# Performance work log

Measured on AMD Instinct MI355X. Metric: run time of the kernel, lower is better.

Reference implementation:

```python
import jax, jax.numpy as jnp
import numpy as np

B, V, S, E, K, FF = 16, 512, 1024, 8, 2, 2048  # batch, n_vars, seq_len, n_experts, top_k, ff_dim


def setup_inputs() -> dict:
    key = jax.random.key(0)
    ks = jax.random.split(key, 6)
    def w(k, shape, fan_in):
        return (jax.random.normal(k, shape, jnp.float32) / np.sqrt(fan_in)).astype(jnp.float32)
    return {
        "x": jax.random.normal(ks[0], (B, S, V), jnp.float32),
        "gate_W": w(ks[1], (E, S), S),          # Gating: Linear(seq_len -> n_experts), no bias
        "exp_W": w(ks[2], (E, S, S), S),        # per-expert Linear(seq_len -> seq_len) weights
        "exp_b": jnp.zeros((E, S), jnp.float32),
        "fc1_W": w(ks[3], (FF, V), V),          # MLPFeat fc1: Linear(n_vars -> ff_dim)
        "fc1_b": jnp.zeros((FF,), jnp.float32),
        "fc2_W": w(ks[4], (V, FF), FF),         # MLPFeat fc2: Linear(ff_dim -> n_vars)
        "fc2_b": jnp.zeros((V,), jnp.float32),
    }


def reference(x, gate_W, exp_W, exp_b, fc1_W, fc1_b, fc2_W, fc2_b):
    # Dropout layers are identity at inference.
    res = x                                   # [B,S,V]
    xt = jnp.swapaxes(x, 1, 2)                # [B,V,S] tokens of dim seq_len

    # --- MLPTime (multi_expert MoE) ---
    logits = jnp.einsum('bvs,es->bve', xt, gate_W)      # [B,V,E]
    probs = jax.nn.softmax(logits, axis=-1)             # gate_logits returned by torch code
    w, sel = jax.lax.top_k(probs, K)                    # [B,V,K]
    # combine top-k weights into a dense per-expert weight [B,V,E] (zeros off top-k)
    full_w = jnp.sum(jax.nn.one_hot(sel, E, dtype=xt.dtype) * w[..., None], axis=2)
    # all-expert outputs, then weighted combine (same math as the per-expert scatter loop)
    all_out = jnp.einsum('bvs,eos->bveo', xt, exp_W) + exp_b[None, None]  # [B,V,E,S]
    moe = jnp.einsum('bve,bveo->bvo', full_w, all_out)                    # [B,V,S]
    t = jax.nn.relu(moe)

    x = jnp.swapaxes(t, 1, 2) + res           # [B,S,V] residual

    # --- MLPFeat ---
    res2 = x
    h = jax.nn.relu(x @ fc1_W.T + fc1_b)      # [B,S,FF]
    x = h @ fc2_W.T + fc2_b + res2            # [B,S,V]
    return (x, probs)
```

## Files before the change

kernel.cpp:

```cpp
#include <hip/hip_runtime.h>
#include <stdint.h>

#define B_  16
#define V_  512
#define S_  1024
#define E_  8
#define FF_ 2048
#define NT_ (B_*V_)
#define NR_ (B_*S_)

typedef __attribute__((ext_vector_type(8))) short bf16x8;
typedef __attribute__((ext_vector_type(4))) float f32x4;

__device__ __forceinline__ unsigned short f2bf(float f) {
    unsigned int u = __float_as_uint(f);
    u += 0x7FFFu + ((u >> 16) & 1u);
    return (unsigned short)(u >> 16);
}
__device__ __forceinline__ float bf2f(unsigned short u) {
    return __uint_as_float(((unsigned int)u) << 16);
}

__device__ __forceinline__ void gl_lds16(const void* g, void* l) {
    __builtin_amdgcn_global_load_lds((const __attribute__((address_space(1))) void*)g,
                                     (__attribute__((address_space(3))) void*)l,
                                     16, 0, 0);
}

__global__ void k_f32_to_bf16(const float* __restrict__ src, unsigned short* __restrict__ dst, int n) {
    int i = (blockIdx.x * blockDim.x + threadIdx.x) * 4;
    if (i + 3 < n) {
        float4 v = *(const float4*)(src + i);
        ushort4 o; o.x = f2bf(v.x); o.y = f2bf(v.y); o.z = f2bf(v.z); o.w = f2bf(v.w);
        *(ushort4*)(dst + i) = o;
    } else {
        for (int j = i; j < n; ++j) dst[j] = f2bf(src[j]);
    }
}

__global__ void k_transpose_xt(const float* __restrict__ x, unsigned short* __restrict__ xt) {
    __shared__ float t[32][33];
    int b = blockIdx.z, st = blockIdx.y, vt = blockIdx.x;
    int col = threadIdx.x & 31, row8 = threadIdx.x >> 5;
    for (int r = 0; r < 4; ++r) {
        int sl = row8 + r * 8;
        t[sl][col] = x[(b * S_ + st * 32 + sl) * V_ + vt * 32 + col];
    }
    __syncthreads();
    for (int r = 0; r < 4; ++r) {
        int vl = row8 + r * 8;
        xt[(size_t)(b * V_ + vt * 32 + vl) * S_ + st * 32 + col] = f2bf(t[col][vl]);
    }
}

__global__ __launch_bounds__(256) void k_gate_part(const float* __restrict__ x,
                                                   const float* __restrict__ gate_W,
                                                   double* __restrict__ part,
                                                   int* __restrict__ cnt) {
    __shared__ float gw[E_ * 128];
    __shared__ double red[4 * 64 * E_];
    int sc = blockIdx.x, vt0 = blockIdx.y * 64, b = blockIdx.z;
    int tid = threadIdx.x;
    if (sc == 0 && blockIdx.y == 0 && b == 0 && tid < E_) cnt[tid] = 0;
    for (int i = tid; i < E_ * 128; i += 256) {
        int e = i >> 7, j = i & 127;
        gw[i] = gate_W[e * S_ + sc * 128 + j];
    }
    __syncthreads();
    int vl = tid & 63, sg = tid >> 6;
    double acc[E_];
    #pragma unroll
    for (int e = 0; e < E_; ++e) acc[e] = 0.0;
    for (int jj = sg; jj < 128; jj += 4) {
        int s = sc * 128 + jj;
        double xv = (double)x[(b * S_ + s) * V_ + vt0 + vl];
        #pragma unroll
        for (int e = 0; e < E_; ++e) acc[e] += xv * (double)gw[e * 128 + jj];
    }
    #pragma unroll
    for (int e = 0; e < E_; ++e) red[(sg * 64 + vl) * E_ + e] = acc[e];
    __syncthreads();
    for (int i = tid; i < 64 * E_; i += 256) {
        int tkn = i >> 3, e = i & 7;
        double s = red[(0 * 64 + tkn) * E_ + e] + red[(1 * 64 + tkn) * E_ + e]
                 + red[(2 * 64 + tkn) * E_ + e] + red[(3 * 64 + tkn) * E_ + e];
        int t = b * V_ + vt0 + tkn;
        part[((size_t)sc * NT_ + t) * E_ + e] = s;
    }
}

__global__ __launch_bounds__(256) void k_gate_fin(const double* __restrict__ part,
                                                  float* __restrict__ probs_out,
                                                  int* __restrict__ cnt, int* __restrict__ tok_of,
                                                  int* __restrict__ tk_slot, float* __restrict__ tk_w) {
    int t = blockIdx.x * 256 + threadIdx.x;
    int lane = threadIdx.x & 63;
    double l[E_];
    #pragma unroll
    for (int e = 0; e < E_; ++e) l[e] = 0.0;
    for (int c = 0; c < S_ / 128; ++c) {
        const double* p = part + ((size_t)c * NT_ + t) * E_;
        #pragma unroll
        for (int e = 0; e < E_; ++e) l[e] += p[e];
    }
    double m = l[0];
    #pragma unroll
    for (int e = 1; e < E_; ++e) m = l[e] > m ? l[e] : m;
    double p[E_], sum = 0.0;
    #pragma unroll
    for (int e = 0; e < E_; ++e) { p[e] = exp(l[e] - m); sum += p[e]; }
    float pf[E_];
    #pragma unroll
    for (int e = 0; e < E_; ++e) pf[e] = (float)(p[e] / sum);
    float4 pa = {pf[0], pf[1], pf[2], pf[3]}, pb = {pf[4], pf[5], pf[6], pf[7]};
    *(float4*)(probs_out + (size_t)t * E_) = pa;
    *(float4*)(probs_out + (size_t)t * E_ + 4) = pb;
    int i0 = 0;
    #pragma unroll
    for (int e = 1; e < E_; ++e) if (pf[e] > pf[i0]) i0 = e;
    int i1 = -1;
    #pragma unroll
    for (int e = 0; e < E_; ++e) if (e != i0 && (i1 < 0 || pf[e] > pf[i1])) i1 = e;
    int sel[2] = {i0, i1};
    float wsel[2] = {pf[i0], pf[i1]};
    #pragma unroll
    for (int k = 0; k < 2; ++k) {
        int ie = sel[k];
        int pos = 0;
        for (int e = 0; e < E_; ++e) {
            unsigned long long msk = __ballot(ie == e);
            if (ie == e) {
                int rank = __popcll(msk & ((1ull << lane) - 1ull));
                int leader = __ffsll((long long)msk) - 1;
                int base = 0;
                if (lane == leader) base = atomicAdd(&cnt[e], __popcll(msk));
                base = __shfl(base, leader);
                pos = base + rank;
            }
        }
        tok_of[ie * NT_ + pos] = t;
        tk_slot[t * 2 + k] = (ie << 16) | pos;
        tk_w[t * 2 + k] = wsel[k];
    }
}

__global__ void k_scan(const int* __restrict__ cnt, int* __restrict__ offs,
                       int* __restrict__ tile_hdr) {
    if (threadIdx.x == 0) {
        int o = 0, nt = 0;
        for (int e = 0; e < E_; ++e) {
            offs[e] = o;
            for (int p = 0; p < cnt[e]; p += 128) {
                tile_hdr[1 + nt * 2] = e;
                tile_hdr[2 + nt * 2] = p;
                ++nt;
            }
            o += cnt[e];
        }
        offs[E_] = o;
        tile_hdr[0] = nt;
    }
}

__device__ __forceinline__ void gemm_k_loop(const unsigned short* a0, const unsigned short* a1,
                                            const unsigned short* b0, const unsigned short* b1,
                                            short* As, short* Bs, int kIters, int wave, int lane,
                                            f32x4 (&acc)[4][4]) {
    char* ldsA = (char*)As + wave * 2048;
    char* ldsB = (char*)Bs + wave * 2048;
    int wm = (wave & 1) << 6, wn = (wave >> 1) << 6;
    int lr = lane & 15, quad = lane >> 4;
    for (int kk = 0; kk < kIters; ++kk) {
        gl_lds16(a0, ldsA);
        gl_lds16(a1, ldsA + 1024);
        gl_lds16(b0, ldsB);
        gl_lds16(b1, ldsB + 1024);
        a0 += 32; a1 += 32; b0 += 32; b1 += 32;
        __syncthreads();
        bf16x8 af[4], bfv[4];
        #pragma unroll
        for (int i = 0; i < 4; ++i)
            af[i] = *(const bf16x8*)(As + (wm + i * 16 + lr) * 32 + quad * 8);
        #pragma unroll
        for (int j = 0; j < 4; ++j)
            bfv[j] = *(const bf16x8*)(Bs + (wn + j * 16 + lr) * 32 + quad * 8);
        #pragma unroll
        for (int i = 0; i < 4; ++i)
            #pragma unroll
            for (int j = 0; j < 4; ++j)
                acc[i][j] = __builtin_amdgcn_mfma_f32_16x16x32_bf16(af[i], bfv[j], acc[i][j], 0, 0, 0);
        __syncthreads();
    }
}

__global__ __launch_bounds__(256) void k_moe_gemm(const unsigned short* __restrict__ xt,
                                                  const unsigned short* __restrict__ expWb,
                                                  const float* __restrict__ exp_b,
                                                  const int* __restrict__ cnt, const int* __restrict__ offs,
                                                  const int* __restrict__ tok_of,
                                                  const int* __restrict__ tile_hdr,
                                                  unsigned short* __restrict__ Yb) {
    int ntl = tile_hdr[0];
    if ((int)blockIdx.x >= ntl) return;
    int e    = tile_hdr[1 + blockIdx.x * 2];
    int pos0 = tile_hdr[2 + blockIdx.x * 2];
    int ne = cnt[e];
    int nt = blockIdx.y;
    __shared__ __align__(16) short As[128 * 32];
    __shared__ __align__(16) short Bs[128 * 32];
    int tid = threadIdx.x, wave = tid >> 6, lane = tid & 63;
    int rA0 = wave * 32 + (lane >> 2);
    int rA1 = rA0 + 16;
    int koff = (lane & 3) * 8;
    int tok0 = tok_of[e * NT_ + min(pos0 + rA0, ne - 1)];
    int tok1 = tok_of[e * NT_ + min(pos0 + rA1, ne - 1)];
    const unsigned short* a0 = xt + (size_t)tok0 * S_ + koff;
    const unsigned short* a1 = xt + (size_t)tok1 * S_ + koff;
    const unsigned short* Wb = expWb + (size_t)e * S_ * S_;
    const unsigned short* b0 = Wb + (size_t)(nt * 128 + rA0) * S_ + koff;
    const unsigned short* b1 = Wb + (size_t)(nt * 128 + rA1) * S_ + koff;
    f32x4 acc[4][4] = {};
    gemm_k_loop(a0, a1, b0, b1, As, Bs, S_ / 32, wave, lane, acc);
    int wm = (wave & 1) << 6, wn = (wave >> 1) << 6;
    int lr = lane & 15, quad = lane >> 4;
    int yrow0 = offs[e];
    #pragma unroll
    for (int i = 0; i < 4; ++i)
        #pragma unroll
        for (int r = 0; r < 4; ++r) {
            int pos = pos0 + wm + i * 16 + quad * 4 + r;
            if (pos < ne) {
                size_t row = (size_t)(yrow0 + pos);
                #pragma unroll
                for (int j = 0; j < 4; ++j) {
                    int col = nt * 128 + wn + j * 16 + lr;
                    Yb[row * S_ + col] = f2bf(acc[i][j][r] + exp_b[e * S_ + col]);
                }
            }
        }
}

__global__ void k_combine(const float* __restrict__ x, const unsigned short* __restrict__ Yb,
                          const int* __restrict__ offs, const int* __restrict__ tk_slot,
                          const float* __restrict__ tk_w,
                          unsigned short* __restrict__ x2b) {
    __shared__ float t[32][33];
    int b = blockIdx.z, st = blockIdx.y, vt = blockIdx.x;
    int tid = threadIdx.x;
    int vl = tid >> 3, sq = (tid & 7) * 4;
    int tok = b * V_ + vt * 32 + vl;
    int s0 = tk_slot[tok * 2 + 0], s1 = tk_slot[tok * 2 + 1];
    float w0 = tk_w[tok * 2 + 0], w1 = tk_w[tok * 2 + 1];
    size_t r0 = (size_t)(offs[s0 >> 16] + (s0 & 0xFFFF));
    size_t r1 = (size_t)(offs[s1 >> 16] + (s1 & 0xFFFF));
    int sg = st * 32 + sq;
    ushort4 y0 = *(const ushort4*)(Yb + r0 * S_ + sg);
    ushort4 y1 = *(const ushort4*)(Yb + r1 * S_ + sg);
    t[vl][sq + 0] = fmaxf(w0 * bf2f(y0.x) + w1 * bf2f(y1.x), 0.f);
    t[vl][sq + 1] = fmaxf(w0 * bf2f(y0.y) + w1 * bf2f(y1.y), 0.f);
    t[vl][sq + 2] = fmaxf(w0 * bf2f(y0.z) + w1 * bf2f(y1.z), 0.f);
    t[vl][sq + 3] = fmaxf(w0 * bf2f(y0.w) + w1 * bf2f(y1.w), 0.f);
    __syncthreads();
    int vcol = tid & 31, srow8 = tid >> 5;
    for (int r = 0; r < 4; ++r) {
        int sl = srow8 + r * 8;
        size_t gi = (size_t)(b * S_ + st * 32 + sl) * V_ + vt * 32 + vcol;
        x2b[gi] = f2bf(x[gi] + t[vcol][sl]);
    }
}

__global__ __launch_bounds__(256) void k_fc1(const unsigned short* __restrict__ x2b,
                                             const unsigned short* __restrict__ w1b,
                                             const float* __restrict__ fc1_b,
                                             unsigned short* __restrict__ h) {
    __shared__ __align__(16) short As[128 * 32];
    __shared__ __align__(16) short Bs[128 * 32];
    int tid = threadIdx.x, wave = tid >> 6, lane = tid & 63;
    int rA0 = wave * 32 + (lane >> 2), rA1 = rA0 + 16;
    int koff = (lane & 3) * 8;
    int m0 = blockIdx.x * 128, n0 = blockIdx.y * 128;
    const unsigned short* a0 = x2b + (size_t)(m0 + rA0) * V_ + koff;
    const unsigned short* a1 = x2b + (size_t)(m0 + rA1) * V_ + koff;
    const unsigned short* b0 = w1b + (size_t)(n0 + rA0) * V_ + koff;
    const unsigned short* b1 = w1b + (size_t)(n0 + rA1) * V_ + koff;
    f32x4 acc[4][4] = {};
    gemm_k_loop(a0, a1, b0, b1, As, Bs, V_ / 32, wave, lane, acc);
    int wm = (wave & 1) << 6, wn = (wave >> 1) << 6;
    int lr = lane & 15, quad = lane >> 4;
    #pragma unroll
    for (int i = 0; i < 4; ++i)
        #pragma unroll
        for (int r = 0; r < 4; ++r) {
            size_t row = (size_t)(m0 + wm + i * 16 + quad * 4 + r);
            #pragma unroll
            for (int j = 0; j < 4; ++j) {
                int col = n0 + wn + j * 16 + lr;
                h[row * FF_ + col] = f2bf(fmaxf(acc[i][j][r] + fc1_b[col], 0.f));
            }
        }
}

__global__ __launch_bounds__(256) void k_fc2(const unsigned short* __restrict__ h,
                                             const unsigned short* __restrict__ w2b,
                                             const float* __restrict__ fc2_b,
                                             const unsigned short* __restrict__ x2b,
                                             float* __restrict__ out) {
    __shared__ __align__(16) short As[128 * 32];
    __shared__ __align__(16) short Bs[128 * 32];
    int tid = threadIdx.x, wave = tid >> 6, lane = tid & 63;
    int rA0 = wave * 32 + (lane >> 2), rA1 = rA0 + 16;
    int koff = (lane & 3) * 8;
    int m0 = blockIdx.x * 128, n0 = blockIdx.y * 128;
    const unsigned short* a0 = h + (size_t)(m0 + rA0) * FF_ + koff;
    const unsigned short* a1 = h + (size_t)(m0 + rA1) * FF_ + koff;
    const unsigned short* b0 = w2b + (size_t)(n0 + rA0) * FF_ + koff;
    const unsigned short* b1 = w2b + (size_t)(n0 + rA1) * FF_ + koff;
    f32x4 acc[4][4] = {};
    gemm_k_loop(a0, a1, b0, b1, As, Bs, FF_ / 32, wave, lane, acc);
    int wm = (wave & 1) << 6, wn = (wave >> 1) << 6;
    int lr = lane & 15, quad = lane >> 4;
    #pragma unroll
    for (int i = 0; i < 4; ++i)
        #pragma unroll
        for (int r = 0; r < 4; ++r) {
            size_t row = (size_t)(m0 + wm + i * 16 + quad * 4 + r);
            #pragma unroll
            for (int j = 0; j < 4; ++j) {
                int col = n0 + wn + j * 16 + lr;
                out[row * V_ + col] = acc[i][j][r] + fc2_b[col] + bf2f(x2b[row * V_ + col]);
            }
        }
}

extern "C" void kernel_launch(void* const* d_in, const int* in_sizes, int n_in,
                              void* d_out, int out_size, void* d_ws, size_t ws_size,
                              hipStream_t stream) {
    const float* x      = (const float*)d_in[0];
    const float* gate_W = (const float*)d_in[1];
    const float* exp_W  = (const float*)d_in[2];
    const float* exp_b  = (const float*)d_in[3];
    const float* fc1_W  = (const float*)d_in[4];
    const float* fc1_b  = (const float*)d_in[5];
    const float* fc2_W  = (const float*)d_in[6];
    const float* fc2_b  = (const float*)d_in[7];
    float* out_x = (float*)d_out;
    float* out_p = (float*)d_out + (size_t)B_ * S_ * V_;

    if (ws_size < (size_t)155582592) return;

    char* ws = (char*)d_ws;
    unsigned short* Yb    = (unsigned short*)(ws);
    unsigned short* xt    = (unsigned short*)(ws +  67108864);
    int*            tile_hdr = (int*)(ws + 83886080);
    unsigned short* x2b   = (unsigned short*)(ws + 117440512);
    unsigned short* expWb = (unsigned short*)(ws + 134217728);
    unsigned short* fc1Wb = (unsigned short*)(ws + 150994944);
    unsigned short* fc2Wb = (unsigned short*)(ws + 153092096);
    char* route = ws + 155189248;
    int*   cnt     = (int*)(route);
    int*   offs    = (int*)(route + 64);
    int*   tok_of  = (int*)(route + 128);
    int*   tk_slot = (int*)(route + 128 + 262144);
    float* tk_w    = (float*)(route + 128 + 262144 + 65536);
    unsigned short* h = (unsigned short*)ws;
    double* part = (double*)ws;

    k_f32_to_bf16<<<dim3(8192), 256, 0, stream>>>(exp_W, expWb, E_ * S_ * S_);
    k_f32_to_bf16<<<dim3(1024), 256, 0, stream>>>(fc1_W, fc1Wb, FF_ * V_);
    k_f32_to_bf16<<<dim3(1024), 256, 0, stream>>>(fc2_W, fc2Wb, V_ * FF_);
    k_transpose_xt<<<dim3(V_ / 32, S_ / 32, B_), 256, 0, stream>>>(x, xt);
    k_gate_part<<<dim3(S_ / 128, V_ / 64, B_), 256, 0, stream>>>(x, gate_W, part, cnt);
    k_gate_fin<<<dim3(NT_ / 256), 256, 0, stream>>>(part, out_p, cnt, tok_of, tk_slot, tk_w);
    k_scan<<<1, 64, 0, stream>>>(cnt, offs, tile_hdr);
    k_moe_gemm<<<dim3(136, S_ / 128), 256, 0, stream>>>(xt, expWb, exp_b, cnt, offs, tok_of, tile_hdr, Yb);
    k_combine<<<dim3(V_ / 32, S_ / 32, B_), 256, 0, stream>>>(x, Yb, offs, tk_slot, tk_w, x2b);
    k_fc1<<<dim3(NR_ / 128, FF_ / 128), 256, 0, stream>>>(x2b, fc1Wb, fc1_b, h);
    k_fc2<<<dim3(NR_ / 128, V_ / 128), 256, 0, stream>>>(h, fc2Wb, fc2_b, x2b, out_x);
}
```

Baseline: 360.3 us.

## Widen MoE and fc1 GEMM tiles to 128x256 and fuse weight conversions

The GEMM k-loop becomes a template on the per-wave N width. The MoE expert GEMM and fc1 now use 128x256 output tiles, with each wave computing 64x128 from 4x8 MFMA accumulators and B-loaders reorganised to match. This raises reuse of the A tile per LDS load and halves the number of blocks that reload activations, at the cost of more accumulator registers, possible lower occupancy and fewer blocks to fill the CUs. The three separate f32-to-bf16 weight conversion launches are merged into one kernel to save launch overhead.

```diff
diff --git a/kernel.cpp b/kernel.cpp
--- a/kernel.cpp
+++ b/kernel.cpp
@@ -27,15 +27,18 @@
                                      16, 0, 0);
 }
 
-__global__ void k_f32_to_bf16(const float* __restrict__ src, unsigned short* __restrict__ dst, int n) {
-    int i = (blockIdx.x * blockDim.x + threadIdx.x) * 4;
-    if (i + 3 < n) {
-        float4 v = *(const float4*)(src + i);
-        ushort4 o; o.x = f2bf(v.x); o.y = f2bf(v.y); o.z = f2bf(v.z); o.w = f2bf(v.w);
-        *(ushort4*)(dst + i) = o;
-    } else {
-        for (int j = i; j < n; ++j) dst[j] = f2bf(src[j]);
-    }
+__device__ __forceinline__ void cvt4(const float* s, unsigned short* d, int i) {
+    float4 v = *(const float4*)(s + i);
+    ushort4 o; o.x = f2bf(v.x); o.y = f2bf(v.y); o.z = f2bf(v.z); o.w = f2bf(v.w);
+    *(ushort4*)(d + i) = o;
+}
+__global__ void k_convert3(const float* __restrict__ s0, unsigned short* __restrict__ d0, int g0,
+                           const float* __restrict__ s1, unsigned short* __restrict__ d1, int g1,
+                           const float* __restrict__ s2, unsigned short* __restrict__ d2) {
+    int g = blockIdx.x * 256 + threadIdx.x;
+    if (g < g0)           cvt4(s0, d0, g * 4);
+    else if (g < g0 + g1) cvt4(s1, d1, (g - g0) * 4);
+    else                  cvt4(s2, d2, (g - g0 - g1) * 4);
 }
 
 __global__ void k_transpose_xt(const float* __restrict__ x, unsigned short* __restrict__ xt) {
@@ -162,32 +165,36 @@
     }
 }
 
-__device__ __forceinline__ void gemm_k_loop(const unsigned short* a0, const unsigned short* a1,
-                                            const unsigned short* b0, const unsigned short* b1,
-                                            short* As, short* Bs, int kIters, int wave, int lane,
-                                            f32x4 (&acc)[4][4]) {
+template<int TN>
+__device__ __forceinline__ void gemm_k_loop_t(const unsigned short* a0, const unsigned short* a1,
+                                              const unsigned short* (&bp)[TN / 2],
+                                              short* As, short* Bs, int kIters, int wave, int lane,
+                                              f32x4 (&acc)[4][TN]) {
     char* ldsA = (char*)As + wave * 2048;
-    char* ldsB = (char*)Bs + wave * 2048;
-    int wm = (wave & 1) << 6, wn = (wave >> 1) << 6;
+    char* ldsB = (char*)Bs + wave * (TN / 2) * 1024;
+    int wm = (wave & 1) << 6;
+    int wn = (wave >> 1) * (TN * 16);
     int lr = lane & 15, quad = lane >> 4;
     for (int kk = 0; kk < kIters; ++kk) {
         gl_lds16(a0, ldsA);
         gl_lds16(a1, ldsA + 1024);
-        gl_lds16(b0, ldsB);
-        gl_lds16(b1, ldsB + 1024);
-        a0 += 32; a1 += 32; b0 += 32; b1 += 32;
+        #pragma unroll
+        for (int c = 0; c < TN / 2; ++c) gl_lds16(bp[c], ldsB + c * 1024);
+        a0 += 32; a1 += 32;
+        #pragma unroll
+        for (int c = 0; c < TN / 2; ++c) bp[c] += 32;
         __syncthreads();
-        bf16x8 af[4], bfv[4];
+        bf16x8 af[4], bfv[TN];
         #pragma unroll
         for (int i = 0; i < 4; ++i)
             af[i] = *(const bf16x8*)(As + (wm + i * 16 + lr) * 32 + quad * 8);
         #pragma unroll
-        for (int j = 0; j < 4; ++j)
+        for (int j = 0; j < TN; ++j)
             bfv[j] = *(const bf16x8*)(Bs + (wn + j * 16 + lr) * 32 + quad * 8);
         #pragma unroll
         for (int i = 0; i < 4; ++i)
             #pragma unroll
-            for (int j = 0; j < 4; ++j)
+            for (int j = 0; j < TN; ++j)
                 acc[i][j] = __builtin_amdgcn_mfma_f32_16x16x32_bf16(af[i], bfv[j], acc[i][j], 0, 0, 0);
         __syncthreads();
     }
@@ -205,9 +212,9 @@
     int e    = tile_hdr[1 + blockIdx.x * 2];
     int pos0 = tile_hdr[2 + blockIdx.x * 2];
     int ne = cnt[e];
-    int nt = blockIdx.y;
+    int n0 = blockIdx.y * 256;
     __shared__ __align__(16) short As[128 * 32];
-    __shared__ __align__(16) short Bs[128 * 32];
+    __shared__ __align__(16) short Bs[256 * 32];
     int tid = threadIdx.x, wave = tid >> 6, lane = tid & 63;
     int rA0 = wave * 32 + (lane >> 2);
     int rA1 = rA0 + 16;
@@ -217,11 +224,13 @@
     const unsigned short* a0 = xt + (size_t)tok0 * S_ + koff;
     const unsigned short* a1 = xt + (size_t)tok1 * S_ + koff;
     const unsigned short* Wb = expWb + (size_t)e * S_ * S_;
-    const unsigned short* b0 = Wb + (size_t)(nt * 128 + rA0) * S_ + koff;
-    const unsigned short* b1 = Wb + (size_t)(nt * 128 + rA1) * S_ + koff;
-    f32x4 acc[4][4] = {};
-    gemm_k_loop(a0, a1, b0, b1, As, Bs, S_ / 32, wave, lane, acc);
-    int wm = (wave & 1) << 6, wn = (wave >> 1) << 6;
+    const unsigned short* bp[4];
+    #pragma unroll
+    for (int c = 0; c < 4; ++c)
+        bp[c] = Wb + (size_t)(n0 + wave * 64 + c * 16 + (lane >> 2)) * S_ + koff;
+    f32x4 acc[4][8] = {};
+    gemm_k_loop_t<8>(a0, a1, bp, As, Bs, S_ / 32, wave, lane, acc);
+    int wm = (wave & 1) << 6, wn = (wave >> 1) << 7;
     int lr = lane & 15, quad = lane >> 4;
     int yrow0 = offs[e];
     #pragma unroll
@@ -232,8 +241,8 @@
             if (pos < ne) {
                 size_t row = (size_t)(yrow0 + pos);
                 #pragma unroll
-                for (int j = 0; j < 4; ++j) {
-                    int col = nt * 128 + wn + j * 16 + lr;
+                for (int j = 0; j < 8; ++j) {
+                    int col = n0 + wn + j * 16 + lr;
                     Yb[row * S_ + col] = f2bf(acc[i][j][r] + exp_b[e * S_ + col]);
                 }
             }
@@ -274,18 +283,20 @@
                                              const float* __restrict__ fc1_b,
                                              unsigned short* __restrict__ h) {
     __shared__ __align__(16) short As[128 * 32];
-    __shared__ __align__(16) short Bs[128 * 32];
+    __shared__ __align__(16) short Bs[256 * 32];
     int tid = threadIdx.x, wave = tid >> 6, lane = tid & 63;
     int rA0 = wave * 32 + (lane >> 2), rA1 = rA0 + 16;
     int koff = (lane & 3) * 8;
-    int m0 = blockIdx.x * 128, n0 = blockIdx.y * 128;
+    int m0 = blockIdx.x * 128, n0 = blockIdx.y * 256;
     const unsigned short* a0 = x2b + (size_t)(m0 + rA0) * V_ + koff;
     const unsigned short* a1 = x2b + (size_t)(m0 + rA1) * V_ + koff;
-    const unsigned short* b0 = w1b + (size_t)(n0 + rA0) * V_ + koff;
-    const unsigned short* b1 = w1b + (size_t)(n0 + rA1) * V_ + koff;
-    f32x4 acc[4][4] = {};
-    gemm_k_loop(a0, a1, b0, b1, As, Bs, V_ / 32, wave, lane, acc);
-    int wm = (wave & 1) << 6, wn = (wave >> 1) << 6;
+    const unsigned short* bp[4];
+    #pragma unroll
+    for (int c = 0; c < 4; ++c)
+        bp[c] = w1b + (size_t)(n0 + wave * 64 + c * 16 + (lane >> 2)) * V_ + koff;
+    f32x4 acc[4][8] = {};
+    gemm_k_loop_t<8>(a0, a1, bp, As, Bs, V_ / 32, wave, lane, acc);
+    int wm = (wave & 1) << 6, wn = (wave >> 1) << 7;
     int lr = lane & 15, quad = lane >> 4;
     #pragma unroll
     for (int i = 0; i < 4; ++i)
@@ -293,7 +304,7 @@
         for (int r = 0; r < 4; ++r) {
             size_t row = (size_t)(m0 + wm + i * 16 + quad * 4 + r);
             #pragma unroll
-            for (int j = 0; j < 4; ++j) {
+            for (int j = 0; j < 8; ++j) {
                 int col = n0 + wn + j * 16 + lr;
                 h[row * FF_ + col] = f2bf(fmaxf(acc[i][j][r] + fc1_b[col], 0.f));
             }
@@ -313,10 +324,12 @@
     int m0 = blockIdx.x * 128, n0 = blockIdx.y * 128;
     const unsigned short* a0 = h + (size_t)(m0 + rA0) * FF_ + koff;
     const unsigned short* a1 = h + (size_t)(m0 + rA1) * FF_ + koff;
-    const unsigned short* b0 = w2b + (size_t)(n0 + rA0) * FF_ + koff;
-    const unsigned short* b1 = w2b + (size_t)(n0 + rA1) * FF_ + koff;
+    const unsigned short* bp[2];
+    #pragma unroll
+    for (int c = 0; c < 2; ++c)
+        bp[c] = w2b + (size_t)(n0 + wave * 32 + c * 16 + (lane >> 2)) * FF_ + koff;
     f32x4 acc[4][4] = {};
-    gemm_k_loop(a0, a1, b0, b1, As, Bs, FF_ / 32, wave, lane, acc);
+    gemm_k_loop_t<4>(a0, a1, bp, As, Bs, FF_ / 32, wave, lane, acc);
     int wm = (wave & 1) << 6, wn = (wave >> 1) << 6;
     int lr = lane & 15, quad = lane >> 4;
     #pragma unroll
@@ -365,15 +378,14 @@
     unsigned short* h = (unsigned short*)ws;
     double* part = (double*)ws;
 
-    k_f32_to_bf16<<<dim3(8192), 256, 0, stream>>>(exp_W, expWb, E_ * S_ * S_);
-    k_f32_to_bf16<<<dim3(1024), 256, 0, stream>>>(fc1_W, fc1Wb, FF_ * V_);
-    k_f32_to_bf16<<<dim3(1024), 256, 0, stream>>>(fc2_W, fc2Wb, V_ * FF_);
+    k_convert3<<<dim3((2097152 + 262144 + 262144) / 256), 256, 0, stream>>>(
+        exp_W, expWb, 2097152, fc1_W, fc1Wb, 262144, fc2_W, fc2Wb);
     k_transpose_xt<<<dim3(V_ / 32, S_ / 32, B_), 256, 0, stream>>>(x, xt);
     k_gate_part<<<dim3(S_ / 128, V_ / 64, B_), 256, 0, stream>>>(x, gate_W, part, cnt);
     k_gate_fin<<<dim3(NT_ / 256), 256, 0, stream>>>(part, out_p, cnt, tok_of, tk_slot, tk_w);
     k_scan<<<1, 64, 0, stream>>>(cnt, offs, tile_hdr);
-    k_moe_gemm<<<dim3(136, S_ / 128), 256, 0, stream>>>(xt, expWb, exp_b, cnt, offs, tok_of, tile_hdr, Yb);
+    k_moe_gemm<<<dim3(135, S_ / 256), 256, 0, stream>>>(xt, expWb, exp_b, cnt, offs, tok_of, tile_hdr, Yb);
     k_combine<<<dim3(V_ / 32, S_ / 32, B_), 256, 0, stream>>>(x, Yb, offs, tk_slot, tk_w, x2b);
-    k_fc1<<<dim3(NR_ / 128, FF_ / 128), 256, 0, stream>>>(x2b, fc1Wb, fc1_b, h);
+    k_fc1<<<dim3(NR_ / 128, FF_ / 256), 256, 0, stream>>>(x2b, fc1Wb, fc1_b, h);
     k_fc2<<<dim3(NR_ / 128, V_ / 128), 256, 0, stream>>>(h, fc2Wb, fc2_b, x2b, out_x);
 }
```

After: 430.8 us. 19.6% more time.

## Switch GEMMs to 32x32x16 MFMA, merge weight conversions, add occupancy hints

Applied to the files above, without the earlier changes.

Replaces the 16x16x32 bf16 MFMA tiling in the shared GEMM inner loop with 32x32x16 MFMAs (2x2 per wave over two k-substeps). The epilogues of the MoE, fc1 and fc2 GEMMs are remapped to the new accumulator layout. The aim is fewer LDS fragment reads per FLOP and higher MFMA throughput. It also fuses the three fp32-to-bf16 weight conversion launches into one kernel, and adds launch_bounds occupancy hints to the MoE and fc1 kernels. The risk is register pressure from 4x16 accumulators under the occupancy hint, plus a changed LDS access pattern that may bank-conflict.

```diff
diff --git a/kernel.cpp b/kernel.cpp
--- a/kernel.cpp
+++ b/kernel.cpp
@@ -10,7 +10,7 @@
 #define NR_ (B_*S_)
 
 typedef __attribute__((ext_vector_type(8))) short bf16x8;
-typedef __attribute__((ext_vector_type(4))) float f32x4;
+typedef __attribute__((ext_vector_type(16))) float f32x16;
 
 __device__ __forceinline__ unsigned short f2bf(float f) {
     unsigned int u = __float_as_uint(f);
@@ -27,15 +27,18 @@
                                      16, 0, 0);
 }
 
-__global__ void k_f32_to_bf16(const float* __restrict__ src, unsigned short* __restrict__ dst, int n) {
-    int i = (blockIdx.x * blockDim.x + threadIdx.x) * 4;
-    if (i + 3 < n) {
-        float4 v = *(const float4*)(src + i);
-        ushort4 o; o.x = f2bf(v.x); o.y = f2bf(v.y); o.z = f2bf(v.z); o.w = f2bf(v.w);
-        *(ushort4*)(dst + i) = o;
-    } else {
-        for (int j = i; j < n; ++j) dst[j] = f2bf(src[j]);
-    }
+__device__ __forceinline__ void cvt4(const float* s, unsigned short* d, int i) {
+    float4 v = *(const float4*)(s + i);
+    ushort4 o; o.x = f2bf(v.x); o.y = f2bf(v.y); o.z = f2bf(v.z); o.w = f2bf(v.w);
+    *(ushort4*)(d + i) = o;
+}
+__global__ void k_convert3(const float* __restrict__ s0, unsigned short* __restrict__ d0, int g0,
+                           const float* __restrict__ s1, unsigned short* __restrict__ d1, int g1,
+                           const float* __restrict__ s2, unsigned short* __restrict__ d2) {
+    int g = blockIdx.x * 256 + threadIdx.x;
+    if (g < g0)           cvt4(s0, d0, g * 4);
+    else if (g < g0 + g1) cvt4(s1, d1, (g - g0) * 4);
+    else                  cvt4(s2, d2, (g - g0 - g1) * 4);
 }
 
 __global__ void k_transpose_xt(const float* __restrict__ x, unsigned short* __restrict__ xt) {
@@ -162,14 +165,14 @@
     }
 }
 
-__device__ __forceinline__ void gemm_k_loop(const unsigned short* a0, const unsigned short* a1,
-                                            const unsigned short* b0, const unsigned short* b1,
-                                            short* As, short* Bs, int kIters, int wave, int lane,
-                                            f32x4 (&acc)[4][4]) {
+__device__ __forceinline__ void gemm_k_loop32(const unsigned short* a0, const unsigned short* a1,
+                                              const unsigned short* b0, const unsigned short* b1,
+                                              short* As, short* Bs, int kIters, int wave, int lane,
+                                              f32x16 (&acc)[2][2]) {
     char* ldsA = (char*)As + wave * 2048;
     char* ldsB = (char*)Bs + wave * 2048;
     int wm = (wave & 1) << 6, wn = (wave >> 1) << 6;
-    int lr = lane & 15, quad = lane >> 4;
+    int l31 = lane & 31, h8 = (lane >> 5) * 8;
     for (int kk = 0; kk < kIters; ++kk) {
         gl_lds16(a0, ldsA);
         gl_lds16(a1, ldsA + 1024);
@@ -177,29 +180,29 @@
         gl_lds16(b1, ldsB + 1024);
         a0 += 32; a1 += 32; b0 += 32; b1 += 32;
         __syncthreads();
-        bf16x8 af[4], bfv[4];
-        #pragma unroll
-        for (int i = 0; i < 4; ++i)
-            af[i] = *(const bf16x8*)(As + (wm + i * 16 + lr) * 32 + quad * 8);
-        #pragma unroll
-        for (int j = 0; j < 4; ++j)
-            bfv[j] = *(const bf16x8*)(Bs + (wn + j * 16 + lr) * 32 + quad * 8);
-        #pragma unroll
-        for (int i = 0; i < 4; ++i)
-            #pragma unroll
-            for (int j = 0; j < 4; ++j)
-                acc[i][j] = __builtin_amdgcn_mfma_f32_16x16x32_bf16(af[i], bfv[j], acc[i][j], 0, 0, 0);
+        #pragma unroll
+        for (int ks = 0; ks < 2; ++ks) {
+            bf16x8 af0 = *(const bf16x8*)(As + (wm + l31) * 32 + ks * 16 + h8);
+            bf16x8 af1 = *(const bf16x8*)(As + (wm + 32 + l31) * 32 + ks * 16 + h8);
+            bf16x8 bg0 = *(const bf16x8*)(Bs + (wn + l31) * 32 + ks * 16 + h8);
+            bf16x8 bg1 = *(const bf16x8*)(Bs + (wn + 32 + l31) * 32 + ks * 16 + h8);
+            acc[0][0] = __builtin_amdgcn_mfma_f32_32x32x16_bf16(af0, bg0, acc[0][0], 0, 0, 0);
+            acc[0][1] = __builtin_amdgcn_mfma_f32_32x32x16_bf16(af0, bg1, acc[0][1], 0, 0, 0);
+            acc[1][0] = __builtin_amdgcn_mfma_f32_32x32x16_bf16(af1, bg0, acc[1][0], 0, 0, 0);
+            acc[1][1] = __builtin_amdgcn_mfma_f32_32x32x16_bf16(af1, bg1, acc[1][1], 0, 0, 0);
+        }
         __syncthreads();
     }
 }
 
-__global__ __launch_bounds__(256) void k_moe_gemm(const unsigned short* __restrict__ xt,
-                                                  const unsigned short* __restrict__ expWb,
-                                                  const float* __restrict__ exp_b,
-                                                  const int* __restrict__ cnt, const int* __restrict__ offs,
-                                                  const int* __restrict__ tok_of,
-                                                  const int* __restrict__ tile_hdr,
-                                                  unsigned short* __restrict__ Yb) {
+
+__global__ __launch_bounds__(256, 4) void k_moe_gemm(const unsigned short* __restrict__ xt,
+                                                     const unsigned short* __restrict__ expWb,
+                                                     const float* __restrict__ exp_b,
+                                                     const int* __restrict__ cnt, const int* __restrict__ offs,
+                                                     const int* __restrict__ tok_of,
+                                                     const int* __restrict__ tile_hdr,
+                                                     unsigned short* __restrict__ Yb) {
     int ntl = tile_hdr[0];
     if ((int)blockIdx.x >= ntl) return;
     int e    = tile_hdr[1 + blockIdx.x * 2];
@@ -219,22 +222,22 @@
     const unsigned short* Wb = expWb + (size_t)e * S_ * S_;
     const unsigned short* b0 = Wb + (size_t)(nt * 128 + rA0) * S_ + koff;
     const unsigned short* b1 = Wb + (size_t)(nt * 128 + rA1) * S_ + koff;
-    f32x4 acc[4][4] = {};
-    gemm_k_loop(a0, a1, b0, b1, As, Bs, S_ / 32, wave, lane, acc);
+    f32x16 acc[2][2] = {};
+    gemm_k_loop32(a0, a1, b0, b1, As, Bs, S_ / 32, wave, lane, acc);
     int wm = (wave & 1) << 6, wn = (wave >> 1) << 6;
-    int lr = lane & 15, quad = lane >> 4;
+    int l31 = lane & 31, half4 = (lane >> 5) * 4;
     int yrow0 = offs[e];
     #pragma unroll
-    for (int i = 0; i < 4; ++i)
-        #pragma unroll
-        for (int r = 0; r < 4; ++r) {
-            int pos = pos0 + wm + i * 16 + quad * 4 + r;
+    for (int mi = 0; mi < 2; ++mi)
+        #pragma unroll
+        for (int reg = 0; reg < 16; ++reg) {
+            int pos = pos0 + wm + mi * 32 + (reg & 3) + 8 * (reg >> 2) + half4;
             if (pos < ne) {
                 size_t row = (size_t)(yrow0 + pos);
                 #pragma unroll
-                for (int j = 0; j < 4; ++j) {
-                    int col = nt * 128 + wn + j * 16 + lr;
-                    Yb[row * S_ + col] = f2bf(acc[i][j][r] + exp_b[e * S_ + col]);
+                for (int nj = 0; nj < 2; ++nj) {
+                    int col = nt * 128 + wn + nj * 32 + l31;
+                    Yb[row * S_ + col] = f2bf(acc[mi][nj][reg] + exp_b[e * S_ + col]);
                 }
             }
         }
@@ -269,10 +272,10 @@
     }
 }
 
-__global__ __launch_bounds__(256) void k_fc1(const unsigned short* __restrict__ x2b,
-                                             const unsigned short* __restrict__ w1b,
-                                             const float* __restrict__ fc1_b,
-                                             unsigned short* __restrict__ h) {
+__global__ __launch_bounds__(256, 4) void k_fc1(const unsigned short* __restrict__ x2b,
+                                                const unsigned short* __restrict__ w1b,
+                                                const float* __restrict__ fc1_b,
+                                                unsigned short* __restrict__ h) {
     __shared__ __align__(16) short As[128 * 32];
     __shared__ __align__(16) short Bs[128 * 32];
     int tid = threadIdx.x, wave = tid >> 6, lane = tid & 63;
@@ -283,19 +286,19 @@
     const unsigned short* a1 = x2b + (size_t)(m0 + rA1) * V_ + koff;
     const unsigned short* b0 = w1b + (size_t)(n0 + rA0) * V_ + koff;
     const unsigned short* b1 = w1b + (size_t)(n0 + rA1) * V_ + koff;
-    f32x4 acc[4][4] = {};
-    gemm_k_loop(a0, a1, b0, b1, As, Bs, V_ / 32, wave, lane, acc);
+    f32x16 acc[2][2] = {};
+    gemm_k_loop32(a0, a1, b0, b1, As, Bs, V_ / 32, wave, lane, acc);
     int wm = (wave & 1) << 6, wn = (wave >> 1) << 6;
-    int lr = lane & 15, quad = lane >> 4;
-    #pragma unroll
-    for (int i = 0; i < 4; ++i)
-        #pragma unroll
-        for (int r = 0; r < 4; ++r) {
-            size_t row = (size_t)(m0 + wm + i * 16 + quad * 4 + r);
+    int l31 = lane & 31, half4 = (lane >> 5) * 4;
+    #pragma unroll
+    for (int mi = 0; mi < 2; ++mi)
+        #pragma unroll
+        for (int reg = 0; reg < 16; ++reg) {
+            size_t row = (size_t)(m0 + wm + mi * 32 + (reg & 3) + 8 * (reg >> 2) + half4);
             #pragma unroll
-            for (int j = 0; j < 4; ++j) {
-                int col = n0 + wn + j * 16 + lr;
-                h[row * FF_ + col] = f2bf(fmaxf(acc[i][j][r] + fc1_b[col], 0.f));
+            for (int nj = 0; nj < 2; ++nj) {
+                int col = n0 + wn + nj * 32 + l31;
+                h[row * FF_ + col] = f2bf(fmaxf(acc[mi][nj][reg] + fc1_b[col], 0.f));
             }
         }
 }
@@ -315,19 +318,19 @@
     const unsigned short* a1 = h + (size_t)(m0 + rA1) * FF_ + koff;
     const unsigned short* b0 = w2b + (size_t)(n0 + rA0) * FF_ + koff;
     const unsigned short* b1 = w2b + (size_t)(n0 + rA1) * FF_ + koff;
-    f32x4 acc[4][4] = {};
-    gemm_k_loop(a0, a1, b0, b1, As, Bs, FF_ / 32, wave, lane, acc);
+    f32x16 acc[2][2] = {};
+    gemm_k_loop32(a0, a1, b0, b1, As, Bs, FF_ / 32, wave, lane, acc);
     int wm = (wave & 1) << 6, wn = (wave >> 1) << 6;
-    int lr = lane & 15, quad = lane >> 4;
-    #pragma unroll
-    for (int i = 0; i < 4; ++i)
-        #pragma unroll
-        for (int r = 0; r < 4; ++r) {
-            size_t row = (size_t)(m0 + wm + i * 16 + quad * 4 + r);
+    int l31 = lane & 31, half4 = (lane >> 5) * 4;
+    #pragma unroll
+    for (int mi = 0; mi < 2; ++mi)
+        #pragma unroll
+        for (int reg = 0; reg < 16; ++reg) {
+            size_t row = (size_t)(m0 + wm + mi * 32 + (reg & 3) + 8 * (reg >> 2) + half4);
             #pragma unroll
-            for (int j = 0; j < 4; ++j) {
-                int col = n0 + wn + j * 16 + lr;
-                out[row * V_ + col] = acc[i][j][r] + fc2_b[col] + bf2f(x2b[row * V_ + col]);
+            for (int nj = 0; nj < 2; ++nj) {
+                int col = n0 + wn + nj * 32 + l31;
+                out[row * V_ + col] = acc[mi][nj][reg] + fc2_b[col] + bf2f(x2b[row * V_ + col]);
             }
         }
 }
@@ -365,9 +368,8 @@
     unsigned short* h = (unsigned short*)ws;
     double* part = (double*)ws;
 
-    k_f32_to_bf16<<<dim3(8192), 256, 0, stream>>>(exp_W, expWb, E_ * S_ * S_);
-    k_f32_to_bf16<<<dim3(1024), 256, 0, stream>>>(fc1_W, fc1Wb, FF_ * V_);
-    k_f32_to_bf16<<<dim3(1024), 256, 0, stream>>>(fc2_W, fc2Wb, V_ * FF_);
+    k_convert3<<<dim3((2097152 + 262144 + 262144) / 256), 256, 0, stream>>>(
+        exp_W, expWb, 2097152, fc1_W, fc1Wb, 262144, fc2_W, fc2Wb);
     k_transpose_xt<<<dim3(V_ / 32, S_ / 32, B_), 256, 0, stream>>>(x, xt);
     k_gate_part<<<dim3(S_ / 128, V_ / 64, B_), 256, 0, stream>>>(x, gate_W, part, cnt);
     k_gate_fin<<<dim3(NT_ / 256), 256, 0, stream>>>(part, out_p, cnt, tok_of, tk_slot, tk_w);
```

Result: slower. 369.4 us (+2.5%).

## Deepen GEMM K-tile to 64 with XOR-swizzled LDS and merge weight conversions

Applied to the files above, without the earlier changes.

All three MFMA GEMMs (MoE, fc1, fc2) now stage a 64-wide K slice per iteration instead of 32. This halves the number of barrier pairs per output tile and issues eight async global-to-LDS loads per step. An XOR swizzle on the 16-byte column groups is meant to avoid LDS bank conflicts on the fragment reads, and a launch-bounds occupancy hint of 3 blocks is added. The three fp32-to-bf16 weight conversion launches are merged into one kernel, at the cost of doubled LDS usage per block.

```diff
diff --git a/kernel.cpp b/kernel.cpp
--- a/kernel.cpp
+++ b/kernel.cpp
@@ -27,15 +27,18 @@
                                      16, 0, 0);
 }
 
-__global__ void k_f32_to_bf16(const float* __restrict__ src, unsigned short* __restrict__ dst, int n) {
-    int i = (blockIdx.x * blockDim.x + threadIdx.x) * 4;
-    if (i + 3 < n) {
-        float4 v = *(const float4*)(src + i);
-        ushort4 o; o.x = f2bf(v.x); o.y = f2bf(v.y); o.z = f2bf(v.z); o.w = f2bf(v.w);
-        *(ushort4*)(dst + i) = o;
-    } else {
-        for (int j = i; j < n; ++j) dst[j] = f2bf(src[j]);
-    }
+__device__ __forceinline__ void cvt4(const float* s, unsigned short* d, int i) {
+    float4 v = *(const float4*)(s + i);
+    ushort4 o; o.x = f2bf(v.x); o.y = f2bf(v.y); o.z = f2bf(v.z); o.w = f2bf(v.w);
+    *(ushort4*)(d + i) = o;
+}
+__global__ void k_convert3(const float* __restrict__ s0, unsigned short* __restrict__ d0, int g0,
+                           const float* __restrict__ s1, unsigned short* __restrict__ d1, int g1,
+                           const float* __restrict__ s2, unsigned short* __restrict__ d2) {
+    int g = blockIdx.x * 256 + threadIdx.x;
+    if (g < g0)           cvt4(s0, d0, g * 4);
+    else if (g < g0 + g1) cvt4(s1, d1, (g - g0) * 4);
+    else                  cvt4(s2, d2, (g - g0 - g1) * 4);
 }
 
 __global__ void k_transpose_xt(const float* __restrict__ x, unsigned short* __restrict__ xt) {
@@ -162,65 +165,77 @@
     }
 }
 
-__device__ __forceinline__ void gemm_k_loop(const unsigned short* a0, const unsigned short* a1,
-                                            const unsigned short* b0, const unsigned short* b1,
-                                            short* As, short* Bs, int kIters, int wave, int lane,
-                                            f32x4 (&acc)[4][4]) {
-    char* ldsA = (char*)As + wave * 2048;
-    char* ldsB = (char*)Bs + wave * 2048;
+__device__ __forceinline__ void gemm_k_loop64(const unsigned short* (&ap)[4],
+                                              const unsigned short* (&bp)[4],
+                                              short* As, short* Bs, int kIters, int wave, int lane,
+                                              f32x4 (&acc)[4][4]) {
+    char* ldsA = (char*)As + wave * 4096;
+    char* ldsB = (char*)Bs + wave * 4096;
     int wm = (wave & 1) << 6, wn = (wave >> 1) << 6;
     int lr = lane & 15, quad = lane >> 4;
+    int pb = (quad ^ (lr & 7)) * 8;
+    const unsigned short* a0 = ap[0]; const unsigned short* a1 = ap[1];
+    const unsigned short* a2 = ap[2]; const unsigned short* a3 = ap[3];
+    const unsigned short* b0 = bp[0]; const unsigned short* b1 = bp[1];
+    const unsigned short* b2 = bp[2]; const unsigned short* b3 = bp[3];
     for (int kk = 0; kk < kIters; ++kk) {
-        gl_lds16(a0, ldsA);
-        gl_lds16(a1, ldsA + 1024);
-        gl_lds16(b0, ldsB);
-        gl_lds16(b1, ldsB + 1024);
-        a0 += 32; a1 += 32; b0 += 32; b1 += 32;
+        gl_lds16(a0, ldsA);        gl_lds16(a1, ldsA + 1024);
+        gl_lds16(a2, ldsA + 2048); gl_lds16(a3, ldsA + 3072);
+        gl_lds16(b0, ldsB);        gl_lds16(b1, ldsB + 1024);
+        gl_lds16(b2, ldsB + 2048); gl_lds16(b3, ldsB + 3072);
+        a0 += 64; a1 += 64; a2 += 64; a3 += 64;
+        b0 += 64; b1 += 64; b2 += 64; b3 += 64;
         __syncthreads();
-        bf16x8 af[4], bfv[4];
-        #pragma unroll
-        for (int i = 0; i < 4; ++i)
-            af[i] = *(const bf16x8*)(As + (wm + i * 16 + lr) * 32 + quad * 8);
-        #pragma unroll
-        for (int j = 0; j < 4; ++j)
-            bfv[j] = *(const bf16x8*)(Bs + (wn + j * 16 + lr) * 32 + quad * 8);
-        #pragma unroll
-        for (int i = 0; i < 4; ++i)
+        #pragma unroll
+        for (int ks = 0; ks < 2; ++ks) {
+            int po = pb ^ (ks << 5);
+            bf16x8 af[4], bfv[4];
+            #pragma unroll
+            for (int i = 0; i < 4; ++i)
+                af[i] = *(const bf16x8*)(As + (wm + i * 16 + lr) * 64 + po);
             #pragma unroll
             for (int j = 0; j < 4; ++j)
-                acc[i][j] = __builtin_amdgcn_mfma_f32_16x16x32_bf16(af[i], bfv[j], acc[i][j], 0, 0, 0);
+                bfv[j] = *(const bf16x8*)(Bs + (wn + j * 16 + lr) * 64 + po);
+            #pragma unroll
+            for (int i = 0; i < 4; ++i)
+                #pragma unroll
+                for (int j = 0; j < 4; ++j)
+                    acc[i][j] = __builtin_amdgcn_mfma_f32_16x16x32_bf16(af[i], bfv[j], acc[i][j], 0, 0, 0);
+        }
         __syncthreads();
     }
 }
 
-__global__ __launch_bounds__(256) void k_moe_gemm(const unsigned short* __restrict__ xt,
-                                                  const unsigned short* __restrict__ expWb,
-                                                  const float* __restrict__ exp_b,
-                                                  const int* __restrict__ cnt, const int* __restrict__ offs,
-                                                  const int* __restrict__ tok_of,
-                                                  const int* __restrict__ tile_hdr,
-                                                  unsigned short* __restrict__ Yb) {
+__global__ __launch_bounds__(256, 3) void k_moe_gemm(const unsigned short* __restrict__ xt,
+                                                     const unsigned short* __restrict__ expWb,
+                                                     const float* __restrict__ exp_b,
+                                                     const int* __restrict__ cnt, const int* __restrict__ offs,
+                                                     const int* __restrict__ tok_of,
+                                                     const int* __restrict__ tile_hdr,
+                                                     unsigned short* __restrict__ Yb) {
     int ntl = tile_hdr[0];
     if ((int)blockIdx.x >= ntl) return;
     int e    = tile_hdr[1 + blockIdx.x * 2];
     int pos0 = tile_hdr[2 + blockIdx.x * 2];
     int ne = cnt[e];
     int nt = blockIdx.y;
-    __shared__ __align__(16) short As[128 * 32];
-    __shared__ __align__(16) short Bs[128 * 32];
+    __shared__ __align__(16) short As[128 * 64];
+    __shared__ __align__(16) short Bs[128 * 64];
     int tid = threadIdx.x, wave = tid >> 6, lane = tid & 63;
-    int rA0 = wave * 32 + (lane >> 2);
-    int rA1 = rA0 + 16;
-    int koff = (lane & 3) * 8;
-    int tok0 = tok_of[e * NT_ + min(pos0 + rA0, ne - 1)];
-    int tok1 = tok_of[e * NT_ + min(pos0 + rA1, ne - 1)];
-    const unsigned short* a0 = xt + (size_t)tok0 * S_ + koff;
-    const unsigned short* a1 = xt + (size_t)tok1 * S_ + koff;
+    int rowLoc = wave * 32 + (lane >> 3);
+    int cg = ((lane & 7) ^ ((lane >> 3) & 7)) * 8;
     const unsigned short* Wb = expWb + (size_t)e * S_ * S_;
-    const unsigned short* b0 = Wb + (size_t)(nt * 128 + rA0) * S_ + koff;
-    const unsigned short* b1 = Wb + (size_t)(nt * 128 + rA1) * S_ + koff;
+    const unsigned short* ap[4];
+    const unsigned short* bp[4];
+    #pragma unroll
+    for (int c = 0; c < 4; ++c) {
+        int rr = rowLoc + c * 8;
+        int tok = tok_of[e * NT_ + min(pos0 + rr, ne - 1)];
+        ap[c] = xt + (size_t)tok * S_ + cg;
+        bp[c] = Wb + (size_t)(nt * 128 + rr) * S_ + cg;
+    }
     f32x4 acc[4][4] = {};
-    gemm_k_loop(a0, a1, b0, b1, As, Bs, S_ / 32, wave, lane, acc);
+    gemm_k_loop64(ap, bp, As, Bs, S_ / 64, wave, lane, acc);
     int wm = (wave & 1) << 6, wn = (wave >> 1) << 6;
     int lr = lane & 15, quad = lane >> 4;
     int yrow0 = offs[e];
@@ -269,22 +284,26 @@
     }
 }
 
-__global__ __launch_bounds__(256) void k_fc1(const unsigned short* __restrict__ x2b,
-                                             const unsigned short* __restrict__ w1b,
-                                             const float* __restrict__ fc1_b,
-                                             unsigned short* __restrict__ h) {
-    __shared__ __align__(16) short As[128 * 32];
-    __shared__ __align__(16) short Bs[128 * 32];
+__global__ __launch_bounds__(256, 3) void k_fc1(const unsigned short* __restrict__ x2b,
+                                                const unsigned short* __restrict__ w1b,
+                                                const float* __restrict__ fc1_b,
+                                                unsigned short* __restrict__ h) {
+    __shared__ __align__(16) short As[128 * 64];
+    __shared__ __align__(16) short Bs[128 * 64];
     int tid = threadIdx.x, wave = tid >> 6, lane = tid & 63;
-    int rA0 = wave * 32 + (lane >> 2), rA1 = rA0 + 16;
-    int koff = (lane & 3) * 8;
+    int rowLoc = wave * 32 + (lane >> 3);
+    int cg = ((lane & 7) ^ ((lane >> 3) & 7)) * 8;
     int m0 = blockIdx.x * 128, n0 = blockIdx.y * 128;
-    const unsigned short* a0 = x2b + (size_t)(m0 + rA0) * V_ + koff;
-    const unsigned short* a1 = x2b + (size_t)(m0 + rA1) * V_ + koff;
-    const unsigned short* b0 = w1b + (size_t)(n0 + rA0) * V_ + koff;
-    const unsigned short* b1 = w1b + (size_t)(n0 + rA1) * V_ + koff;
+    const unsigned short* ap[4];
+    const unsigned short* bp[4];
+    #pragma unroll
+    for (int c = 0; c < 4; ++c) {
+        int rr = rowLoc + c * 8;
+        ap[c] = x2b + (size_t)(m0 + rr) * V_ + cg;
+        bp[c] = w1b + (size_t)(n0 + rr) * V_ + cg;
+    }
     f32x4 acc[4][4] = {};
-    gemm_k_loop(a0, a1, b0, b1, As, Bs, V_ / 32, wave, lane, acc);
+    gemm_k_loop64(ap, bp, As, Bs, V_ / 64, wave, lane, acc);
     int wm = (wave & 1) << 6, wn = (wave >> 1) << 6;
     int lr = lane & 15, quad = lane >> 4;
     #pragma unroll
@@ -300,23 +319,27 @@
         }
 }
 
-__global__ __launch_bounds__(256) void k_fc2(const unsigned short* __restrict__ h,
-                                             const unsigned short* __restrict__ w2b,
-                                             const float* __restrict__ fc2_b,
-                                             const unsigned short* __restrict__ x2b,
-                                             float* __restrict__ out) {
-    __shared__ __align__(16) short As[128 * 32];
-    __shared__ __align__(16) short Bs[128 * 32];
+__global__ __launch_bounds__(256, 3) void k_fc2(const unsigned short* __restrict__ h,
+                                                const unsigned short* __restrict__ w2b,
+                                                const float* __restrict__ fc2_b,
+                                                const unsigned short* __restrict__ x2b,
+                                                float* __restrict__ out) {
+    __shared__ __align__(16) short As[128 * 64];
+    __shared__ __align__(16) short Bs[128 * 64];
     int tid = threadIdx.x, wave = tid >> 6, lane = tid & 63;
-    int rA0 = wave * 32 + (lane >> 2), rA1 = rA0 + 16;
-    int koff = (lane & 3) * 8;
+    int rowLoc = wave * 32 + (lane >> 3);
+    int cg = ((lane & 7) ^ ((lane >> 3) & 7)) * 8;
     int m0 = blockIdx.x * 128, n0 = blockIdx.y * 128;
-    const unsigned short* a0 = h + (size_t)(m0 + rA0) * FF_ + koff;
-    const unsigned short* a1 = h + (size_t)(m0 + rA1) * FF_ + koff;
-    const unsigned short* b0 = w2b + (size_t)(n0 + rA0) * FF_ + koff;
-    const unsigned short* b1 = w2b + (size_t)(n0 + rA1) * FF_ + koff;
+    const unsigned short* ap[4];
+    const unsigned short* bp[4];
+    #pragma unroll
+    for (int c = 0; c < 4; ++c) {
+        int rr = rowLoc + c * 8;
+        ap[c] = h + (size_t)(m0 + rr) * FF_ + cg;
+        bp[c] = w2b + (size_t)(n0 + rr) * FF_ + cg;
+    }
     f32x4 acc[4][4] = {};
-    gemm_k_loop(a0, a1, b0, b1, As, Bs, FF_ / 32, wave, lane, acc);
+    gemm_k_loop64(ap, bp, As, Bs, FF_ / 64, wave, lane, acc);
     int wm = (wave & 1) << 6, wn = (wave >> 1) << 6;
     int lr = lane & 15, quad = lane >> 4;
     #pragma unroll
@@ -365,9 +388,8 @@
     unsigned short* h = (unsigned short*)ws;
     double* part = (double*)ws;
 
-    k_f32_to_bf16<<<dim3(8192), 256, 0, stream>>>(exp_W, expWb, E_ * S_ * S_);
-    k_f32_to_bf16<<<dim3(1024), 256, 0, stream>>>(fc1_W, fc1Wb, FF_ * V_);
-    k_f32_to_bf16<<<dim3(1024), 256, 0, stream>>>(fc2_W, fc2Wb, V_ * FF_);
+    k_convert3<<<dim3((2097152 + 262144 + 262144) / 256), 256, 0, stream>>>(
+        exp_W, expWb, 2097152, fc1_W, fc1Wb, 262144, fc2_W, fc2Wb);
     k_transpose_xt<<<dim3(V_ / 32, S_ / 32, B_), 256, 0, stream>>>(x, xt);
     k_gate_part<<<dim3(S_ / 128, V_ / 64, B_), 256, 0, stream>>>(x, gate_W, part, cnt);
     k_gate_fin<<<dim3(NT_ / 256), 256, 0, stream>>>(part, out_p, cnt, tok_of, tk_slot, tk_w);
```

Measured after the change: 343.0 us. 4.8% less time.
